# Kernel tuning notes

Measured on AMD Instinct MI355X. Metric: run time of the kernel, lower is better.

Reference implementation:

```python
import jax, jax.numpy as jnp
import numpy as np

OUT = 7          # pooler output_size
RATIO = 2        # sampling_ratio
MIN_LEVEL, MAX_LEVEL = 2, 5
CANON_SIZE, CANON_LEVEL = 224.0, 4.0
SCALES = (0.25, 0.125, 0.0625, 0.03125)


def setup_inputs() -> dict:
    key = jax.random.key(0)
    ks = jax.random.split(key, 8)
    feat2 = jax.random.normal(ks[0], (2, 256, 200, 304), dtype=jnp.float32)
    feat3 = jax.random.normal(ks[1], (2, 256, 100, 152), dtype=jnp.float32)
    feat4 = jax.random.normal(ks[2], (2, 256, 50, 76), dtype=jnp.float32)
    feat5 = jax.random.normal(ks[3], (2, 256, 25, 38), dtype=jnp.float32)
    M = 1000
    imH, imW = 800.0, 1216.0
    cx = jax.random.uniform(ks[4], (M,)) * imW
    cy = jax.random.uniform(ks[5], (M,)) * imH
    wh = jax.random.uniform(ks[6], (M, 2)) * 400.0 + 8.0  # box sizes 8..408 px -> spans levels 2..5
    x0 = jnp.clip(cx - wh[:, 0] / 2, 0.0, imW - 1.0)
    x1 = jnp.clip(cx + wh[:, 0] / 2, 1.0, imW)
    y0 = jnp.clip(cy - wh[:, 1] / 2, 0.0, imH - 1.0)
    y1 = jnp.clip(cy + wh[:, 1] / 2, 1.0, imH)
    boxes = jnp.stack([x0, y0, x1, y1], axis=1).astype(jnp.float32)
    batch_idx = jax.random.randint(ks[7], (M,), 0, 2, dtype=jnp.int32)
    return {"feat2": feat2, "feat3": feat3, "feat4": feat4, "feat5": feat5,
            "boxes": boxes, "batch_idx": batch_idx}


def _assign_levels(boxes):
    # detectron2 assign_boxes_to_levels
    area = (boxes[:, 2] - boxes[:, 0]) * (boxes[:, 3] - boxes[:, 1])
    size = jnp.sqrt(area)
    lvl = jnp.floor(CANON_LEVEL + jnp.log2(size / CANON_SIZE + 1e-8))
    lvl = jnp.clip(lvl, MIN_LEVEL, MAX_LEVEL)
    return (lvl - MIN_LEVEL).astype(jnp.int32)  # [M] in 0..3


def _axis_weights(c, size):
    # torchvision roi_align bilinear clamping (per axis, separable)
    valid = ((c >= -1.0) & (c <= size)).astype(c.dtype)
    cc = jnp.maximum(c, 0.0)
    lo_f = jnp.floor(cc)
    cap = lo_f >= size - 1
    lo = jnp.where(cap, size - 1, lo_f).astype(jnp.int32)
    hi = jnp.where(cap, size - 1, lo + 1).astype(jnp.int32)
    l = jnp.where(cap, 0.0, cc - lo_f)
    return lo, hi, (1.0 - l) * valid, l * valid


def _roi_align(feat, boxes, bidx, scale):
    # feat [N,C,H,W], boxes [M,4] xyxy, aligned=True (ROIAlignV2)
    N, C, H, W = feat.shape
    M = boxes.shape[0]
    b = boxes * scale - 0.5  # aligned: shift by -0.5 after scaling
    x0, y0 = b[:, 0], b[:, 1]
    bin_w = (b[:, 2] - x0) / OUT
    bin_h = (b[:, 3] - y0) / OUT
    S = OUT * RATIO
    s = np.arange(S)
    offs = jnp.asarray((s // RATIO) + ((s % RATIO) + 0.5) / RATIO, dtype=feat.dtype)  # [S]
    ys = y0[:, None] + bin_h[:, None] * offs[None, :]  # [M,S]
    xs = x0[:, None] + bin_w[:, None] * offs[None, :]  # [M,S]
    ylo, yhi, wyl, wyh = _axis_weights(ys, H)
    xlo, xhi, wxl, wxh = _axis_weights(xs, W)

    def gather(yi, xi):
        # -> [M, S, S, C]
        return feat[bidx[:, None, None], :, yi[:, :, None], xi[:, None, :]]

    val = (gather(ylo, xlo) * (wyl[:, :, None] * wxl[:, None, :])[..., None]
         + gather(ylo, xhi) * (wyl[:, :, None] * wxh[:, None, :])[..., None]
         + gather(yhi, xlo) * (wyh[:, :, None] * wxl[:, None, :])[..., None]
         + gather(yhi, xhi) * (wyh[:, :, None] * wxh[:, None, :])[..., None])
    # average over the RATIOxRATIO sample subgrid of each output bin
    val = val.reshape(M, OUT, RATIO, OUT, RATIO, C).mean(axis=(2, 4))
    return val.transpose(0, 3, 1, 2)  # [M, C, OUT, OUT]


def reference(feat2, feat3, feat4, feat5, boxes, batch_idx):
    feats = (feat2, feat3, feat4, feat5)
    assign = _assign_levels(boxes)  # [M]
    M, C = boxes.shape[0], feat2.shape[1]
    out = jnp.zeros((M, C, OUT, OUT), dtype=feat2.dtype)
    for lvl, (f, sc) in enumerate(zip(feats, SCALES)):
        pooled = _roi_align(f, boxes, batch_idx, sc)
        out = out + pooled * (assign == lvl)[:, None, None, None].astype(out.dtype)
    return out
```

## Files before the change

### kernel.cpp

```cpp
#include <hip/hip_runtime.h>


#define NCH 256
#define POOL 7
#define NBIN 49
#define CAP 1152
#define WPB 4
#define TS 128

typedef __attribute__((address_space(3))) void       as3_void;
typedef __attribute__((address_space(1))) const void as1_void;

__global__ __launch_bounds__(256) void roi_precompute_kernel(
    const float* __restrict__ boxes, const int* __restrict__ bidx,
    unsigned int* __restrict__ tab, int M)
{
    const int lane = threadIdx.x & 63;
    const int m = blockIdx.x * WPB + (threadIdx.x >> 6);
    if (m >= M) return;

    float bx0 = boxes[4 * m + 0];
    float by0 = boxes[4 * m + 1];
    float bx1 = boxes[4 * m + 2];
    float by1 = boxes[4 * m + 3];

    float area = (bx1 - bx0) * (by1 - by0);
    float sz   = sqrtf(area);
    float lvlf = floorf(4.0f + log2f(sz / 224.0f + 1e-8f));
    lvlf = fminf(fmaxf(lvlf, 2.0f), 5.0f);
    int lvl = (int)lvlf - 2;

    int H, W; float scale;
    if (lvl == 0)      { H = 200; W = 304; scale = 0.25f;    }
    else if (lvl == 1) { H = 100; W = 152; scale = 0.125f;   }
    else if (lvl == 2) { H = 50;  W = 76;  scale = 0.0625f;  }
    else               { H = 25;  W = 38;  scale = 0.03125f; }

    float x0 = bx0 * scale - 0.5f;
    float y0 = by0 * scale - 0.5f;
    float bin_w = (bx1 * scale - 0.5f - x0) * (1.0f / 7.0f);
    float bin_h = (by1 * scale - 0.5f - y0) * (1.0f / 7.0f);

    int axis = lane >= 14;
    int s    = axis ? (lane - 14) : lane;
    float off = (float)(s >> 1) + ((s & 1) ? 0.75f : 0.25f);
    float cv    = axis ? (y0 + bin_h * off) : (x0 + bin_w * off);
    float size  = axis ? (float)H : (float)W;
    float valid = (cv >= -1.0f && cv <= size) ? 1.0f : 0.0f;
    float cc    = fmaxf(cv, 0.0f);
    float lo_f  = floorf(cc);
    bool  capd  = lo_f >= size - 1.0f;
    int   lo    = capd ? (int)size - 1 : (int)lo_f;
    int   hi    = capd ? lo : lo + 1;
    float l     = capd ? 0.0f : (cc - lo_f);
    float wlo   = (1.0f - l) * valid;
    float whi   = l * valid;

    int rx0 = __shfl(lo, 0);
    int rxe = __shfl(hi, 13);
    int ry0 = __shfl(lo, 14);
    int rye = __shfl(hi, 27);

    int FW  = rxe - rx0 + 1;
    int FH  = rye - ry0 + 1;
    int lpr = (FW + 3) >> 2;
    int RS4 = lpr << 2;
    int rpi = 64 / lpr;
    int iters = (FH + rpi - 1) / rpi;
    unsigned Mg  = (65536u   + (unsigned)lpr - 1u) / (unsigned)lpr;
    unsigned Mg2 = (4194304u + (unsigned)RS4 - 1u) / (unsigned)RS4;
    unsigned HW  = (unsigned)(H * W);
    unsigned base_off = (unsigned)bidx[m] * 256u * HW
                      + (unsigned)ry0 * (unsigned)W + (unsigned)rx0;
    int FH2 = FH;
    if (FH2 * RS4 > CAP) FH2 = CAP / RS4;
    unsigned lastoff = base_off + 255u * HW
                     + (unsigned)(FH - 1) * (unsigned)W + (unsigned)RS4;
    int safe = (lastoff <= 2u * 256u * HW) && (FH * RS4 <= CAP);

    unsigned* t = tab + (size_t)m * TS;
    if (lane == 0) {
        t[0]  = base_off;
        t[1]  = (unsigned)lvl;
        t[2]  = HW;
        t[3]  = (unsigned)W;
        t[4]  = (unsigned)lpr;
        t[5]  = Mg;
        t[6]  = (unsigned)rpi;
        t[7]  = (unsigned)iters;
        t[8]  = (unsigned)(rpi * W);
        t[9]  = (unsigned)((rpi * RS4) << 2);
        t[10] = (unsigned)((FH - 1) * W);
        t[11] = (unsigned)safe;
        t[12] = (unsigned)FW;
        t[13] = (unsigned)RS4;
        t[14] = (unsigned)FH2;
        t[15] = Mg2;
    }
    if (lane < 28) {
        if (!axis) {
            int xr = lo - rx0;
            int xp = min(xr + 1, FW - 1);
            uint4 v;
            v.x = (unsigned)xr;
            v.y = (unsigned)xp;
            v.z = __float_as_uint(wlo);
            v.w = __float_as_uint(whi);
            *(uint4*)(t + 16 + 4 * s) = v;
        } else {
            uint4 v;
            v.x = (unsigned)((lo - ry0) * RS4);
            v.y = (unsigned)((hi - ry0) * RS4);
            v.z = __float_as_uint(wlo);
            v.w = __float_as_uint(whi);
            *(uint4*)(t + 72 + 4 * s) = v;
        }
    }
}

__global__ __launch_bounds__(256, 4) void roi_align_kernel(
    const float* __restrict__ f0, const float* __restrict__ f1,
    const float* __restrict__ f2, const float* __restrict__ f3,
    const unsigned int* __restrict__ tab,
    float* __restrict__ out, int M)
{
    __shared__ float sF[WPB][2 * CAP];

    const int lane = threadIdx.x & 63;
    const int w    = __builtin_amdgcn_readfirstlane(threadIdx.x >> 6);

    const unsigned mblocks = (unsigned)gridDim.x >> 7;
    const unsigned rb    = blockIdx.x;
    const unsigned xcd   = rb & 7u;
    const unsigned idx   = rb >> 3;
    const unsigned cpblk = idx / mblocks;
    const unsigned mb    = idx - cpblk * mblocks;
    const int c0 = (int)((xcd * 16u + cpblk) * 2u);
    const int m  = (int)(mb * WPB) + w;
    if (m >= M) return;

    const unsigned* t = tab + (size_t)m * TS;

    const int ci = lane < NBIN ? lane : 0;
    const int py = ci / POOL;
    const int px = ci - POOL * py;
    const uint4* xt = (const uint4*)(t + 16);
    const uint4* yt = (const uint4*)(t + 72);
    const uint4 X0 = xt[2 * px];
    const uint4 X1 = xt[2 * px + 1];
    const uint4 Y0 = yt[2 * py];
    const uint4 Y1 = yt[2 * py + 1];

    const uint4 s0 = *(const uint4*)(t);
    const uint4 s1 = *(const uint4*)(t + 4);
    const uint4 s2 = *(const uint4*)(t + 8);

    const int lvl = __builtin_amdgcn_readfirstlane((int)s0.y);
    const float* fp = (lvl == 0) ? f0 : (lvl == 1) ? f1 : (lvl == 2) ? f2 : f3;
    const unsigned HW = s0.z;
    const unsigned Wd = s0.w;
    const float* srcA = fp + (size_t)(s0.x + (unsigned)c0 * HW);
    const float* srcB = srcA + HW;

    const int safe = __builtin_amdgcn_readfirstlane((int)s2.w);
    if (safe) {
        const int lpr      = __builtin_amdgcn_readfirstlane((int)s1.x);
        const unsigned Mg  = s1.y;
        const int rpi      = __builtin_amdgcn_readfirstlane((int)s1.z);
        const int iters    = __builtin_amdgcn_readfirstlane((int)s1.w);
        const unsigned gstep  = s2.x;
        const unsigned lstepB = __builtin_amdgcn_readfirstlane((int)s2.y);
        const unsigned fhw    = s2.z;

        int sfy  = (int)(((unsigned)lane * Mg) >> 16);
        int sfx4 = (lane - sfy * lpr) << 2;
        if (sfy < rpi) {
            const float* gA    = srcA + (unsigned)sfy * Wd + (unsigned)sfx4;
            const float* gmaxA = srcA + fhw + (unsigned)sfx4;
            const float* gB    = srcB + (unsigned)sfy * Wd + (unsigned)sfx4;
            const float* gmaxB = srcB + fhw + (unsigned)sfx4;
            char* lbA = (char*)&sF[w][0];
            char* lbB = (char*)&sF[w][CAP];
            for (int it = 0; it < iters; ++it) {
                const float* gcA = (gA > gmaxA) ? gmaxA : gA;
                const float* gcB = (gB > gmaxB) ? gmaxB : gB;
                __builtin_amdgcn_global_load_lds((as1_void*)gcA,
                                                 (as3_void*)lbA, 16, 0, 0);
                __builtin_amdgcn_global_load_lds((as1_void*)gcB,
                                                 (as3_void*)lbB, 16, 0, 0);
                gA += gstep; gB += gstep;
                lbA += lstepB; lbB += lstepB;
            }
        }
    } else {
        const uint4 s3 = *(const uint4*)(t + 12);
        const int FW  = __builtin_amdgcn_readfirstlane((int)s3.x);
        const int RS4 = __builtin_amdgcn_readfirstlane((int)s3.y);
        const int FH2 = __builtin_amdgcn_readfirstlane((int)s3.z);
        const unsigned Mg2 = s3.w;
        const int tot = FH2 * RS4;
        for (int i = lane; i < tot; i += 64) {
            int fy = (int)(((unsigned)i * Mg2) >> 22);
            int fx = i - fy * RS4;
            int cx = fx < FW ? fx : FW - 1;
            unsigned goff = (unsigned)fy * Wd + (unsigned)cx;
            sF[w][i]       = srcA[goff];
            sF[w][CAP + i] = srcB[goff];
        }
    }

    __builtin_amdgcn_s_waitcnt(0);
    __asm__ __volatile__("" ::: "memory");

    if (lane < NBIN) {
        const float* FbA = &sF[w][0];
        const float* FbB = &sF[w][CAP];
        const unsigned xr0 = X0.x, xp0 = X0.y, xr1 = X1.x, xp1 = X1.y;
        const float wxl0 = __uint_as_float(X0.z), wxh0 = __uint_as_float(X0.w);
        const float wxl1 = __uint_as_float(X1.z), wxh1 = __uint_as_float(X1.w);
        const unsigned ra = Y0.x, rb2 = Y0.y, rc = Y1.x, rd = Y1.y;
        const float wy0 = __uint_as_float(Y0.z), wy1 = __uint_as_float(Y0.w);
        const float wy2 = __uint_as_float(Y1.z), wy3 = __uint_as_float(Y1.w);

        float a0 = FbA[ra + xr0] * wxl0 + FbA[ra + xp0] * wxh0
                 + FbA[ra + xr1] * wxl1 + FbA[ra + xp1] * wxh1;
        float a1 = FbA[rb2 + xr0] * wxl0 + FbA[rb2 + xp0] * wxh0
                 + FbA[rb2 + xr1] * wxl1 + FbA[rb2 + xp1] * wxh1;
        float a2 = FbA[rc + xr0] * wxl0 + FbA[rc + xp0] * wxh0
                 + FbA[rc + xr1] * wxl1 + FbA[rc + xp1] * wxh1;
        float a3 = FbA[rd + xr0] * wxl0 + FbA[rd + xp0] * wxh0
                 + FbA[rd + xr1] * wxl1 + FbA[rd + xp1] * wxh1;
        float accA = wy0 * a0 + wy1 * a1 + wy2 * a2 + wy3 * a3;

        float b0 = FbB[ra + xr0] * wxl0 + FbB[ra + xp0] * wxh0
                 + FbB[ra + xr1] * wxl1 + FbB[ra + xp1] * wxh1;
        float b1 = FbB[rb2 + xr0] * wxl0 + FbB[rb2 + xp0] * wxh0
                 + FbB[rb2 + xr1] * wxl1 + FbB[rb2 + xp1] * wxh1;
        float b2 = FbB[rc + xr0] * wxl0 + FbB[rc + xp0] * wxh0
                 + FbB[rc + xr1] * wxl1 + FbB[rc + xp1] * wxh1;
        float b3 = FbB[rd + xr0] * wxl0 + FbB[rd + xp0] * wxh0
                 + FbB[rd + xr1] * wxl1 + FbB[rd + xp1] * wxh1;
        float accB = wy0 * b0 + wy1 * b1 + wy2 * b2 + wy3 * b3;

        size_t ob = ((size_t)m * NCH + (unsigned)c0) * NBIN + (unsigned)lane;
        out[ob]        = accA * 0.25f;
        out[ob + NBIN] = accB * 0.25f;
    }
}

extern "C" void kernel_launch(void* const* d_in, const int* in_sizes, int n_in,
                              void* d_out, int out_size, void* d_ws, size_t ws_size,
                              hipStream_t stream) {
    const float* f0    = (const float*)d_in[0];
    const float* f1    = (const float*)d_in[1];
    const float* f2    = (const float*)d_in[2];
    const float* f3    = (const float*)d_in[3];
    const float* boxes = (const float*)d_in[4];
    const int*   bidx  = (const int*)d_in[5];
    float* out = (float*)d_out;

    int M = in_sizes[4] / 4;
    unsigned int* tab = (unsigned int*)d_ws;

    int pblocks = (M + WPB - 1) / WPB;
    hipLaunchKernelGGL(roi_precompute_kernel, dim3(pblocks), dim3(256), 0,
                       stream, boxes, bidx, tab, M);

    int mblocks = (M + WPB - 1) / WPB;
    int blocks = mblocks * (NCH / 2);
    hipLaunchKernelGGL(roi_align_kernel, dim3(blocks), dim3(256), 0, stream,
                       f0, f1, f2, f3, tab, out, M);
}
```

Measured before the change: 276.0 us.

## Register-staged ROI tile loads, 2-wave blocks, and separate direct-gather fallback kernel

Replaces the async global-to-LDS copies with unrolled vector loads into registers that are then stored to shared memory, capped at a fixed number of iterations. Blocks shrink from four to two waves, which halves the shared memory per block and lets more blocks be resident. ROIs whose footprint does not fit, or that need too many iterations, are added to a list with an atomic counter. A new fallback kernel handles them by gathering straight from global memory. This adds a memset, a third launch, and more registers in exchange for simpler per-wave loading and fewer wave-level stalls.

```diff
diff --git a/kernel.cpp b/kernel.cpp
--- a/kernel.cpp
+++ b/kernel.cpp
@@ -5,18 +5,22 @@
 #define POOL 7
 #define NBIN 49
 #define CAP 1152
-#define WPB 4
-#define TS 128
-
-typedef __attribute__((address_space(3))) void       as3_void;
-typedef __attribute__((address_space(1))) const void as1_void;
+#define WPB 2
+#define PWPB 4
+#define TS 160
+#define ITMAX 5
+
+typedef float f4g __attribute__((ext_vector_type(4), aligned(4)));
+typedef float f4l __attribute__((ext_vector_type(4), aligned(16)));
+#define RFL(x) __builtin_amdgcn_readfirstlane(x)
 
 __global__ __launch_bounds__(256) void roi_precompute_kernel(
     const float* __restrict__ boxes, const int* __restrict__ bidx,
-    unsigned int* __restrict__ tab, int M)
+    unsigned int* __restrict__ tab, unsigned int* __restrict__ list,
+    unsigned int* __restrict__ cnt, int M)
 {
     const int lane = threadIdx.x & 63;
-    const int m = blockIdx.x * WPB + (threadIdx.x >> 6);
+    const int m = blockIdx.x * PWPB + (threadIdx.x >> 6);
     if (m >= M) return;
 
     float bx0 = boxes[4 * m + 0];
@@ -67,16 +71,13 @@
     int RS4 = lpr << 2;
     int rpi = 64 / lpr;
     int iters = (FH + rpi - 1) / rpi;
-    unsigned Mg  = (65536u   + (unsigned)lpr - 1u) / (unsigned)lpr;
-    unsigned Mg2 = (4194304u + (unsigned)RS4 - 1u) / (unsigned)RS4;
+    unsigned Mg  = (65536u + (unsigned)lpr - 1u) / (unsigned)lpr;
     unsigned HW  = (unsigned)(H * W);
     unsigned base_off = (unsigned)bidx[m] * 256u * HW
                       + (unsigned)ry0 * (unsigned)W + (unsigned)rx0;
-    int FH2 = FH;
-    if (FH2 * RS4 > CAP) FH2 = CAP / RS4;
-    unsigned lastoff = base_off + 255u * HW
-                     + (unsigned)(FH - 1) * (unsigned)W + (unsigned)RS4;
-    int safe = (lastoff <= 2u * 256u * HW) && (FH * RS4 <= CAP);
+    int safe = (iters * rpi * RS4 <= CAP)
+            && (iters <= ITMAX)
+            && (FW <= W - 4);
 
     unsigned* t = tab + (size_t)m * TS;
     if (lane == 0) {
@@ -89,13 +90,17 @@
         t[6]  = (unsigned)rpi;
         t[7]  = (unsigned)iters;
         t[8]  = (unsigned)(rpi * W);
-        t[9]  = (unsigned)((rpi * RS4) << 2);
+        t[9]  = 0u;
         t[10] = (unsigned)((FH - 1) * W);
         t[11] = (unsigned)safe;
         t[12] = (unsigned)FW;
         t[13] = (unsigned)RS4;
-        t[14] = (unsigned)FH2;
-        t[15] = Mg2;
+        t[14] = 0u;
+        t[15] = 0u;
+        if (!safe) {
+            unsigned i = atomicAdd(cnt, 1u);
+            list[i] = (unsigned)m;
+        }
     }
     if (lane < 28) {
         if (!axis) {
@@ -114,11 +119,15 @@
             v.z = __float_as_uint(wlo);
             v.w = __float_as_uint(whi);
             *(uint4*)(t + 72 + 4 * s) = v;
+            uint2 vw;
+            vw.x = (unsigned)((lo - ry0) * W);
+            vw.y = (unsigned)((hi - ry0) * W);
+            *(uint2*)(t + 128 + 2 * s) = vw;
         }
     }
 }
 
-__global__ __launch_bounds__(256, 4) void roi_align_kernel(
+__global__ __launch_bounds__(128, 4) void roi_align_kernel(
     const float* __restrict__ f0, const float* __restrict__ f1,
     const float* __restrict__ f2, const float* __restrict__ f3,
     const unsigned int* __restrict__ tab,
@@ -155,96 +164,160 @@
     const uint4 s1 = *(const uint4*)(t + 4);
     const uint4 s2 = *(const uint4*)(t + 8);
 
-    const int lvl = __builtin_amdgcn_readfirstlane((int)s0.y);
+    const int safe = RFL((int)s2.w);
+    if (!safe) return;
+
+    const int lvl = RFL((int)s0.y);
     const float* fp = (lvl == 0) ? f0 : (lvl == 1) ? f1 : (lvl == 2) ? f2 : f3;
     const unsigned HW = s0.z;
     const unsigned Wd = s0.w;
-    const float* srcA = fp + (size_t)(s0.x + (unsigned)c0 * HW);
-    const float* srcB = srcA + HW;
-
-    const int safe = __builtin_amdgcn_readfirstlane((int)s2.w);
-    if (safe) {
-        const int lpr      = __builtin_amdgcn_readfirstlane((int)s1.x);
-        const unsigned Mg  = s1.y;
-        const int rpi      = __builtin_amdgcn_readfirstlane((int)s1.z);
-        const int iters    = __builtin_amdgcn_readfirstlane((int)s1.w);
-        const unsigned gstep  = s2.x;
-        const unsigned lstepB = __builtin_amdgcn_readfirstlane((int)s2.y);
-        const unsigned fhw    = s2.z;
-
-        int sfy  = (int)(((unsigned)lane * Mg) >> 16);
-        int sfx4 = (lane - sfy * lpr) << 2;
-        if (sfy < rpi) {
-            const float* gA    = srcA + (unsigned)sfy * Wd + (unsigned)sfx4;
-            const float* gmaxA = srcA + fhw + (unsigned)sfx4;
-            const float* gB    = srcB + (unsigned)sfy * Wd + (unsigned)sfx4;
-            const float* gmaxB = srcB + fhw + (unsigned)sfx4;
-            char* lbA = (char*)&sF[w][0];
-            char* lbB = (char*)&sF[w][CAP];
-            for (int it = 0; it < iters; ++it) {
-                const float* gcA = (gA > gmaxA) ? gmaxA : gA;
-                const float* gcB = (gB > gmaxB) ? gmaxB : gB;
-                __builtin_amdgcn_global_load_lds((as1_void*)gcA,
-                                                 (as3_void*)lbA, 16, 0, 0);
-                __builtin_amdgcn_global_load_lds((as1_void*)gcB,
-                                                 (as3_void*)lbB, 16, 0, 0);
-                gA += gstep; gB += gstep;
-                lbA += lstepB; lbB += lstepB;
+    const unsigned baseA = s0.x + (unsigned)c0 * HW;
+
+    const int lpr      = RFL((int)s1.x);
+    const unsigned Mg  = s1.y;
+    const int rpi      = RFL((int)s1.z);
+    const int iters    = RFL((int)s1.w);
+    const unsigned gstep = s2.x;
+    const unsigned fhw   = s2.z;
+    const int RS4 = lpr << 2;
+
+    const int sfy  = (int)(((unsigned)lane * Mg) >> 16);
+    const int sfx4 = (lane - sfy * lpr) << 2;
+    const bool act = sfy < rpi;
+
+    f4g a[ITMAX], b[ITMAX];
+    {
+        unsigned off = baseA + (unsigned)sfy * Wd + (unsigned)sfx4;
+        const unsigned ocap = baseA + fhw + (unsigned)sfx4;
+        #pragma unroll
+        for (int it = 0; it < ITMAX; ++it) {
+            if (act && it < iters) {
+                unsigned o = off < ocap ? off : ocap;
+                a[it] = *(const f4g*)(fp + o);
+                b[it] = *(const f4g*)(fp + o + HW);
             }
-        }
-    } else {
-        const uint4 s3 = *(const uint4*)(t + 12);
-        const int FW  = __builtin_amdgcn_readfirstlane((int)s3.x);
-        const int RS4 = __builtin_amdgcn_readfirstlane((int)s3.y);
-        const int FH2 = __builtin_amdgcn_readfirstlane((int)s3.z);
-        const unsigned Mg2 = s3.w;
-        const int tot = FH2 * RS4;
-        for (int i = lane; i < tot; i += 64) {
-            int fy = (int)(((unsigned)i * Mg2) >> 22);
-            int fx = i - fy * RS4;
-            int cx = fx < FW ? fx : FW - 1;
-            unsigned goff = (unsigned)fy * Wd + (unsigned)cx;
-            sF[w][i]       = srcA[goff];
-            sF[w][CAP + i] = srcB[goff];
-        }
-    }
-
-    __builtin_amdgcn_s_waitcnt(0);
-    __asm__ __volatile__("" ::: "memory");
-
-    if (lane < NBIN) {
+            off += gstep;
+        }
+    }
+    {
+        float* LA = &sF[w][0];
+        unsigned lo = (unsigned)sfy * (unsigned)RS4 + (unsigned)sfx4;
+        const unsigned lstep = (unsigned)(rpi * RS4);
+        #pragma unroll
+        for (int it = 0; it < ITMAX; ++it) {
+            if (act && it < iters) {
+                *(f4l*)(LA + lo)       = a[it];
+                *(f4l*)(LA + CAP + lo) = b[it];
+            }
+            lo += lstep;
+        }
+    }
+
+    {
         const float* FbA = &sF[w][0];
         const float* FbB = &sF[w][CAP];
-        const unsigned xr0 = X0.x, xp0 = X0.y, xr1 = X1.x, xp1 = X1.y;
+        const unsigned xA = X0.x, xB = X1.x;
         const float wxl0 = __uint_as_float(X0.z), wxh0 = __uint_as_float(X0.w);
         const float wxl1 = __uint_as_float(X1.z), wxh1 = __uint_as_float(X1.w);
         const unsigned ra = Y0.x, rb2 = Y0.y, rc = Y1.x, rd = Y1.y;
         const float wy0 = __uint_as_float(Y0.z), wy1 = __uint_as_float(Y0.w);
         const float wy2 = __uint_as_float(Y1.z), wy3 = __uint_as_float(Y1.w);
 
-        float a0 = FbA[ra + xr0] * wxl0 + FbA[ra + xp0] * wxh0
-                 + FbA[ra + xr1] * wxl1 + FbA[ra + xp1] * wxh1;
-        float a1 = FbA[rb2 + xr0] * wxl0 + FbA[rb2 + xp0] * wxh0
-                 + FbA[rb2 + xr1] * wxl1 + FbA[rb2 + xp1] * wxh1;
-        float a2 = FbA[rc + xr0] * wxl0 + FbA[rc + xp0] * wxh0
-                 + FbA[rc + xr1] * wxl1 + FbA[rc + xp1] * wxh1;
-        float a3 = FbA[rd + xr0] * wxl0 + FbA[rd + xp0] * wxh0
-                 + FbA[rd + xr1] * wxl1 + FbA[rd + xp1] * wxh1;
+        const float* r0 = FbA + ra;
+        const float* r1 = FbA + rb2;
+        const float* r2 = FbA + rc;
+        const float* r3 = FbA + rd;
+        float a0 = r0[xA] * wxl0 + r0[xA + 1] * wxh0
+                 + r0[xB] * wxl1 + r0[xB + 1] * wxh1;
+        float a1 = r1[xA] * wxl0 + r1[xA + 1] * wxh0
+                 + r1[xB] * wxl1 + r1[xB + 1] * wxh1;
+        float a2 = r2[xA] * wxl0 + r2[xA + 1] * wxh0
+                 + r2[xB] * wxl1 + r2[xB + 1] * wxh1;
+        float a3 = r3[xA] * wxl0 + r3[xA + 1] * wxh0
+                 + r3[xB] * wxl1 + r3[xB + 1] * wxh1;
         float accA = wy0 * a0 + wy1 * a1 + wy2 * a2 + wy3 * a3;
 
-        float b0 = FbB[ra + xr0] * wxl0 + FbB[ra + xp0] * wxh0
-                 + FbB[ra + xr1] * wxl1 + FbB[ra + xp1] * wxh1;
-        float b1 = FbB[rb2 + xr0] * wxl0 + FbB[rb2 + xp0] * wxh0
-                 + FbB[rb2 + xr1] * wxl1 + FbB[rb2 + xp1] * wxh1;
-        float b2 = FbB[rc + xr0] * wxl0 + FbB[rc + xp0] * wxh0
-                 + FbB[rc + xr1] * wxl1 + FbB[rc + xp1] * wxh1;
-        float b3 = FbB[rd + xr0] * wxl0 + FbB[rd + xp0] * wxh0
-                 + FbB[rd + xr1] * wxl1 + FbB[rd + xp1] * wxh1;
+        const float* q0 = FbB + ra;
+        const float* q1 = FbB + rb2;
+        const float* q2 = FbB + rc;
+        const float* q3 = FbB + rd;
+        float b0 = q0[xA] * wxl0 + q0[xA + 1] * wxh0
+                 + q0[xB] * wxl1 + q0[xB + 1] * wxh1;
+        float b1 = q1[xA] * wxl0 + q1[xA + 1] * wxh0
+                 + q1[xB] * wxl1 + q1[xB + 1] * wxh1;
+        float b2 = q2[xA] * wxl0 + q2[xA + 1] * wxh0
+                 + q2[xB] * wxl1 + q2[xB + 1] * wxh1;
+        float b3 = q3[xA] * wxl0 + q3[xA + 1] * wxh0
+                 + q3[xB] * wxl1 + q3[xB + 1] * wxh1;
         float accB = wy0 * b0 + wy1 * b1 + wy2 * b2 + wy3 * b3;
 
-        size_t ob = ((size_t)m * NCH + (unsigned)c0) * NBIN + (unsigned)lane;
-        out[ob]        = accA * 0.25f;
-        out[ob + NBIN] = accB * 0.25f;
+        if (lane < NBIN) {
+            size_t ob = ((size_t)m * NCH + (unsigned)c0) * NBIN
+                      + (unsigned)lane;
+            out[ob]        = accA * 0.25f;
+            out[ob + NBIN] = accB * 0.25f;
+        }
+    }
+}
+
+__global__ __launch_bounds__(256) void roi_fallback_kernel(
+    const float* __restrict__ f0, const float* __restrict__ f1,
+    const float* __restrict__ f2, const float* __restrict__ f3,
+    const unsigned int* __restrict__ tab, const unsigned int* __restrict__ list,
+    const unsigned int* __restrict__ cnt,
+    float* __restrict__ out, int M)
+{
+    const int lane = threadIdx.x & 63;
+    const unsigned wv = blockIdx.x * 4u + (threadIdx.x >> 6);
+    const unsigned nw = gridDim.x * 4u;
+    const unsigned total = cnt[0] * 256u;
+
+    const int ci = lane < NBIN ? lane : 0;
+    const int py = ci / POOL;
+    const int px = ci - POOL * py;
+
+    for (unsigned u = wv; u < total; u += nw) {
+        const unsigned mi = list[u >> 8];
+        const unsigned c  = u & 255u;
+        const unsigned* t = tab + (size_t)mi * TS;
+
+        const uint4 s0 = *(const uint4*)(t);
+        const int lvl = (int)s0.y;
+        const float* fp = (lvl == 0) ? f0 : (lvl == 1) ? f1
+                        : (lvl == 2) ? f2 : f3;
+        const float* src = fp + (size_t)(s0.x + c * s0.z);
+
+        const uint4* xt = (const uint4*)(t + 16);
+        const uint4* yt = (const uint4*)(t + 72);
+        const uint2* yw = (const uint2*)(t + 128);
+        const uint4 X0 = xt[2 * px];
+        const uint4 X1 = xt[2 * px + 1];
+        const uint4 Y0 = yt[2 * py];
+        const uint4 Y1 = yt[2 * py + 1];
+        const uint2 W0 = yw[2 * py];
+        const uint2 W1 = yw[2 * py + 1];
+
+        const unsigned xr0 = X0.x, xp0 = X0.y, xr1 = X1.x, xp1 = X1.y;
+        const float wxl0 = __uint_as_float(X0.z), wxh0 = __uint_as_float(X0.w);
+        const float wxl1 = __uint_as_float(X1.z), wxh1 = __uint_as_float(X1.w);
+        const unsigned ra = W0.x, rb = W0.y, rc = W1.x, rd = W1.y;
+        const float wy0 = __uint_as_float(Y0.z), wy1 = __uint_as_float(Y0.w);
+        const float wy2 = __uint_as_float(Y1.z), wy3 = __uint_as_float(Y1.w);
+
+        float a0 = src[ra + xr0] * wxl0 + src[ra + xp0] * wxh0
+                 + src[ra + xr1] * wxl1 + src[ra + xp1] * wxh1;
+        float a1 = src[rb + xr0] * wxl0 + src[rb + xp0] * wxh0
+                 + src[rb + xr1] * wxl1 + src[rb + xp1] * wxh1;
+        float a2 = src[rc + xr0] * wxl0 + src[rc + xp0] * wxh0
+                 + src[rc + xr1] * wxl1 + src[rc + xp1] * wxh1;
+        float a3 = src[rd + xr0] * wxl0 + src[rd + xp0] * wxh0
+                 + src[rd + xr1] * wxl1 + src[rd + xp1] * wxh1;
+        float acc = wy0 * a0 + wy1 * a1 + wy2 * a2 + wy3 * a3;
+
+        if (lane < NBIN) {
+            size_t ob = ((size_t)mi * NCH + c) * NBIN + (unsigned)lane;
+            out[ob] = acc * 0.25f;
+        }
     }
 }
 
@@ -260,14 +333,21 @@
     float* out = (float*)d_out;
 
     int M = in_sizes[4] / 4;
-    unsigned int* tab = (unsigned int*)d_ws;
-
-    int pblocks = (M + WPB - 1) / WPB;
+    unsigned int* cnt  = (unsigned int*)d_ws;
+    unsigned int* list = cnt + 64;
+    unsigned int* tab  = cnt + 64 + 8192;
+
+    hipMemsetAsync(d_ws, 0, 4, stream);
+
+    int pblocks = (M + PWPB - 1) / PWPB;
     hipLaunchKernelGGL(roi_precompute_kernel, dim3(pblocks), dim3(256), 0,
-                       stream, boxes, bidx, tab, M);
+                       stream, boxes, bidx, tab, list, cnt, M);
 
     int mblocks = (M + WPB - 1) / WPB;
     int blocks = mblocks * (NCH / 2);
-    hipLaunchKernelGGL(roi_align_kernel, dim3(blocks), dim3(256), 0, stream,
+    hipLaunchKernelGGL(roi_align_kernel, dim3(blocks), dim3(128), 0, stream,
                        f0, f1, f2, f3, tab, out, M);
+
+    hipLaunchKernelGGL(roi_fallback_kernel, dim3(128), dim3(256), 0, stream,
+                       f0, f1, f2, f3, tab, list, cnt, out, M);
 }
```

Result: slower. 322.9 us (+17.0%).
